# Optimization experiments

Hardware: AMD Instinct MI355X
Metric: run time of the kernel (lower is better)

## Reference

```python
import jax, jax.numpy as jnp
import numpy as np

B, INPUTS, HIDDEN, OUTPUTS = 128, 512, 512, 512
MAXLEN = INPUTS  # required by the module's bmm/cat shape constraints


def setup_inputs() -> dict:
    key = jax.random.key(0)
    ks = jax.random.split(key, 11)
    s = 0.03
    return {
        "x": jax.random.normal(ks[0], (B, INPUTS, MAXLEN), jnp.float32),
        "attn_W": jax.random.normal(ks[1], (MAXLEN, HIDDEN + INPUTS), jnp.float32) * s,
        "attn_b": jax.random.normal(ks[2], (MAXLEN,), jnp.float32) * s,
        "comb_W": jax.random.normal(ks[3], (HIDDEN, INPUTS + MAXLEN), jnp.float32) * s,
        "comb_b": jax.random.normal(ks[4], (HIDDEN,), jnp.float32) * s,
        "w_ih": jax.random.normal(ks[5], (3 * HIDDEN, HIDDEN), jnp.float32) * s,
        "w_hh": jax.random.normal(ks[6], (3 * HIDDEN, HIDDEN), jnp.float32) * s,
        "b_ih": jax.random.normal(ks[7], (3 * HIDDEN,), jnp.float32) * s,
        "b_hh": jax.random.normal(ks[8], (3 * HIDDEN,), jnp.float32) * s,
        "out_W": jax.random.normal(ks[9], (OUTPUTS, HIDDEN), jnp.float32) * s,
        "out_b": jax.random.normal(ks[10], (OUTPUTS,), jnp.float32) * s,
    }


def reference(x, attn_W, attn_b, comb_W, comb_b, w_ih, w_hh, b_ih, b_hh, out_W, out_b):
    # x: [B, inputs, T] with T == max_length == inputs (shape constraint of the module).
    # The torch code loops over batch with identical per-element math -> vectorize over B,
    # and uses lax.scan over the sequential time dimension.
    Bn = x.shape[0]
    H = w_hh.shape[1]
    xs = jnp.moveaxis(x, 2, 0)  # [T, B, inputs]
    h0 = jnp.zeros((Bn, H), x.dtype)

    def step(h, inp):
        # inp: [B, inputs], h: [B, hidden]
        cat = jnp.concatenate([inp, h], axis=1)                     # [B, inputs+hidden]
        attn_w = jax.nn.softmax(cat @ attn_W.T + attn_b, axis=1)    # [B, max_length]
        applied = jnp.einsum('bm,bmt->bt', attn_w, x)               # [B, T]
        g = jnp.concatenate([inp, applied], axis=1) @ comb_W.T + comb_b
        g = jax.nn.relu(g)                                          # [B, hidden]
        # PyTorch GRU cell
        gi = g @ w_ih.T + b_ih
        gh = h @ w_hh.T + b_hh
        ir, iz, i_n = jnp.split(gi, 3, axis=1)
        hr, hz, h_n = jnp.split(gh, 3, axis=1)
        r = jax.nn.sigmoid(ir + hr)
        z = jax.nn.sigmoid(iz + hz)
        n = jnp.tanh(i_n + r * h_n)
        h_new = (1.0 - z) * n + z * h
        return h_new, None

    h_final, _ = jax.lax.scan(step, h0, xs)
    return h_final @ out_W.T + out_b  # [B, outputs]
```

## Files before the change

### kernel.cpp

```cpp
#include <hip/hip_runtime.h>


typedef unsigned short u16;
typedef unsigned int u32;
typedef _Float16 h2 __attribute__((ext_vector_type(2)));
typedef _Float16 f16x8 __attribute__((ext_vector_type(8)));
typedef float f32x4 __attribute__((ext_vector_type(4)));
typedef float f32x2 __attribute__((ext_vector_type(2)));
typedef u32 u32x4 __attribute__((ext_vector_type(4)));

#define MAGIC 0x13579BDFu

#define OFF_AW   65536
#define OFF_CW   1114112
#define OFF_WIH  2162688
#define OFF_WHH  3735552
#define OFF_OW   5308416
#define OFF_HB   5832704
#define OFF_SF   5963776
#define OFF_AP0  6225920
#define OFF_AP1  6488064
#define OFF_GB   6750208
#define OFF_GH   6881280
#define OFF_XT   7667712
#define WS_NEED  74776576

#define FS_S   64
#define FS_C   96
#define FS_G   128
#define FS_GH  160
#define FS_H   192
#define FS_RDY 224

__device__ __forceinline__ float sigmoidf_(float v) { return 1.f / (1.f + __expf(-v)); }
__device__ __forceinline__ float tanhf_(float v) {
  v = fminf(fmaxf(v, -15.f), 15.f);
  float e2 = __expf(2.f * v);
  return (e2 - 1.f) / (e2 + 1.f);
}
__device__ __forceinline__ u32 packh2(float a, float b) {
  h2 v; v.x = (_Float16)a; v.y = (_Float16)b;
  return __builtin_bit_cast(u32, v);
}

__device__ __forceinline__ void vm_drain() { asm volatile("s_waitcnt vmcnt(0)" ::: "memory"); }

__device__ __forceinline__ f32x2 ldg_f32x2(const void* p) {
  f32x2 r;
  asm volatile("global_load_dwordx2 %0, %1, off sc0 sc1\n\ts_waitcnt vmcnt(0)"
               : "=v"(r) : "v"(p) : "memory");
  return r;
}
__device__ __forceinline__ void ldg4x16_off(const void* p, u32x4& a, u32x4& b, u32x4& c, u32x4& d) {
  asm volatile(
      "global_load_dwordx4 %0, %4, off sc0 sc1\n\t"
      "global_load_dwordx4 %1, %4, off offset:16 sc0 sc1\n\t"
      "global_load_dwordx4 %2, %4, off offset:32 sc0 sc1\n\t"
      "global_load_dwordx4 %3, %4, off offset:48 sc0 sc1\n\t"
      "s_waitcnt vmcnt(0)"
      : "=&v"(a), "=&v"(b), "=&v"(c), "=&v"(d)
      : "v"(p) : "memory");
}
__device__ __forceinline__ void ldg_ap16(const float* pa, const float* pb,
                                         u32x4 (&A)[8], u32x4 (&B)[8]) {
  asm volatile(
      "global_load_dwordx4 %0, %16, off sc0 sc1\n\t"
      "global_load_dwordx4 %1, %16, off offset:16 sc0 sc1\n\t"
      "global_load_dwordx4 %2, %16, off offset:32 sc0 sc1\n\t"
      "global_load_dwordx4 %3, %16, off offset:48 sc0 sc1\n\t"
      "global_load_dwordx4 %4, %16, off offset:64 sc0 sc1\n\t"
      "global_load_dwordx4 %5, %16, off offset:80 sc0 sc1\n\t"
      "global_load_dwordx4 %6, %16, off offset:96 sc0 sc1\n\t"
      "global_load_dwordx4 %7, %16, off offset:112 sc0 sc1\n\t"
      "global_load_dwordx4 %8, %17, off sc0 sc1\n\t"
      "global_load_dwordx4 %9, %17, off offset:16 sc0 sc1\n\t"
      "global_load_dwordx4 %10, %17, off offset:32 sc0 sc1\n\t"
      "global_load_dwordx4 %11, %17, off offset:48 sc0 sc1\n\t"
      "global_load_dwordx4 %12, %17, off offset:64 sc0 sc1\n\t"
      "global_load_dwordx4 %13, %17, off offset:80 sc0 sc1\n\t"
      "global_load_dwordx4 %14, %17, off offset:96 sc0 sc1\n\t"
      "global_load_dwordx4 %15, %17, off offset:112 sc0 sc1\n\t"
      "s_waitcnt vmcnt(0)"
      : "=&v"(A[0]), "=&v"(A[1]), "=&v"(A[2]), "=&v"(A[3]),
        "=&v"(A[4]), "=&v"(A[5]), "=&v"(A[6]), "=&v"(A[7]),
        "=&v"(B[0]), "=&v"(B[1]), "=&v"(B[2]), "=&v"(B[3]),
        "=&v"(B[4]), "=&v"(B[5]), "=&v"(B[6]), "=&v"(B[7])
      : "v"(pa), "v"(pb) : "memory");
}
__device__ __forceinline__ void ldg_gh12(const float* q0, const float* q1,
                                         const float* q2, const float* q3,
                                         float (&rr)[4], float (&zz)[4], float (&nn)[4]) {
  asm volatile(
      "global_load_dword %0, %12, off offset:-2048 sc0 sc1\n\t"
      "global_load_dword %4, %12, off sc0 sc1\n\t"
      "global_load_dword %8, %12, off offset:2048 sc0 sc1\n\t"
      "global_load_dword %1, %13, off offset:-2048 sc0 sc1\n\t"
      "global_load_dword %5, %13, off sc0 sc1\n\t"
      "global_load_dword %9, %13, off offset:2048 sc0 sc1\n\t"
      "global_load_dword %2, %14, off offset:-2048 sc0 sc1\n\t"
      "global_load_dword %6, %14, off sc0 sc1\n\t"
      "global_load_dword %10, %14, off offset:2048 sc0 sc1\n\t"
      "global_load_dword %3, %15, off offset:-2048 sc0 sc1\n\t"
      "global_load_dword %7, %15, off sc0 sc1\n\t"
      "global_load_dword %11, %15, off offset:2048 sc0 sc1\n\t"
      "s_waitcnt vmcnt(0)"
      : "=&v"(rr[0]), "=&v"(rr[1]), "=&v"(rr[2]), "=&v"(rr[3]),
        "=&v"(zz[0]), "=&v"(zz[1]), "=&v"(zz[2]), "=&v"(zz[3]),
        "=&v"(nn[0]), "=&v"(nn[1]), "=&v"(nn[2]), "=&v"(nn[3])
      : "v"(q0), "v"(q1), "v"(q2), "v"(q3) : "memory");
}

__device__ __forceinline__ void stg_f32(float* p, float v) {
  asm volatile("global_store_dword %0, %1, off sc0 sc1" :: "v"(p), "v"(v) : "memory");
}
__device__ __forceinline__ void stg_f32x2(float* p, f32x2 v) {
  asm volatile("global_store_dwordx2 %0, %1, off sc0 sc1" :: "v"(p), "v"(v) : "memory");
}
__device__ __forceinline__ void stg_u16(u16* p, u32 v) {
  asm volatile("global_store_short %0, %1, off sc0 sc1" :: "v"(p), "v"(v) : "memory");
}

__device__ __forceinline__ void flag_add(u32* ctrl, int fs) {
  vm_drain();
  __syncthreads();
  if (threadIdx.x == 0) atomicAdd(ctrl + fs, 1u);
}
__device__ __forceinline__ void flag_wait_ge(u32* ctrl, int fs, u32 target, int warp) {
  if (warp == 0) {
    u32 v;
    do {
      v = __hip_atomic_load(ctrl + fs, __ATOMIC_RELAXED, __HIP_MEMORY_SCOPE_AGENT);
    } while (v < target);
  }
  __syncthreads();
}

__device__ __forceinline__ void stage_rows(const u16* gsrc, char* lds, int tid) {
  const int row = tid >> 4, c = tid & 15;
  const u16* g = gsrc + row * 512 + c * 32;
  u32x4 a, b, cc, d;
  ldg4x16_off(g, a, b, cc, d);
  u32x4* dst = (u32x4*)(lds + row * 1040 + c * 64);
  dst[0] = a; dst[1] = b; dst[2] = cc; dst[3] = d;
}

#define MFMA(a, b, c) __builtin_amdgcn_mfma_f32_16x16x32_f16((a), (b), (c), 0, 0, 0)

extern "C" __global__ void __launch_bounds__(256, 1)
rnn_fused(const float* __restrict__ x, const float* __restrict__ attn_W,
          const float* __restrict__ attn_b, const float* __restrict__ comb_W,
          const float* __restrict__ comb_b, const float* __restrict__ w_ih,
          const float* __restrict__ w_hh, const float* __restrict__ b_ih,
          const float* __restrict__ b_hh, const float* __restrict__ out_W,
          const float* __restrict__ out_b, float* __restrict__ out,
          char* __restrict__ ws)
{
  const int tid  = threadIdx.x;
  const int lane = tid & 63;
  const int warp = tid >> 6;

  int team, tb;
  {
    const int r = blockIdx.x & 7;
    const int s = blockIdx.x >> 3;
    if (s < 16) {
      if (r < 4) { team = r * 2 + (s >> 3); tb = s & 7; }
      else       { team = (r - 4) * 2 + (s >> 3); tb = 8 + (s & 7); }
    } else {
      team = r; tb = s;
    }
  }

  const int tt   = tb * 256 + tid;
  const int gb0  = team * 16;
  const int lb   = tb >> 1;
  const int half = tb & 1;
  const int b    = gb0 + lb;
  const int m0h  = half * 256;

  u32* ctrl = (u32*)ws + team * 1024;

  u16*   AW  = (u16*)(ws + OFF_AW);
  u16*   CW  = (u16*)(ws + OFF_CW);
  u16*   WIH = (u16*)(ws + OFF_WIH);
  u16*   WHH = (u16*)(ws + OFF_WHH);
  u16*   OW  = (u16*)(ws + OFF_OW);
  u16*   HB  = (u16*)(ws + OFF_HB);
  float* Sf  = (float*)(ws + OFF_SF);
  float* AP0 = (float*)(ws + OFF_AP0);
  float* AP1 = (float*)(ws + OFF_AP1);
  u16*   GB  = (u16*)(ws + OFF_GB);
  float* GH  = (float*)(ws + OFF_GH);
  u16*   XT  = (u16*)(ws + OFF_XT);

  __shared__ char smem[16704];
  float*     tbuf   = (float*)smem;
  u32*       pLDS   = (u32*)smem;
  float*     redbuf = (float*)(smem + 512);
  float*     rbuf   = (float*)(smem + 8704);
  _Float16*  ldsF   = (_Float16*)smem;

  if (tb == 0) {
    for (int i = 1 + tid; i < 1024; i += 256) ctrl[i] = 0u;
    __syncthreads();
    if (tid == 0) { __threadfence(); atomicExch(ctrl, MAGIC); }
  }
  if (tid == 0) {
    while (__hip_atomic_load(ctrl, __ATOMIC_RELAXED, __HIP_MEMORY_SCOPE_AGENT) != MAGIC) {}
    __threadfence();
  }
  __syncthreads();

  for (int i = tt; i < 512 * 1024; i += 8192) AW[i]  = __builtin_bit_cast(u16, (_Float16)attn_W[i]);
  for (int i = tt; i < 512 * 1024; i += 8192) CW[i]  = __builtin_bit_cast(u16, (_Float16)comb_W[i]);
  for (int i = tt; i < 1536 * 512; i += 8192) WIH[i] = __builtin_bit_cast(u16, (_Float16)w_ih[i]);
  for (int i = tt; i < 1536 * 512; i += 8192) WHH[i] = __builtin_bit_cast(u16, (_Float16)w_hh[i]);
  for (int i = tt; i < 512 * 512;  i += 8192) OW[i]  = __builtin_bit_cast(u16, (_Float16)out_W[i]);
  HB[(size_t)gb0 * 512 + tt] = 0;

  {
    const float* xb  = x  + (size_t)b * 512 * 512;
    u16*         xtB = XT + (size_t)b * 512 * 512;
    for (int mt = 0; mt < 4; ++mt) {
      for (int ct = 0; ct < 8; ++ct) {
        for (int rr = warp; rr < 64; rr += 4)
          tbuf[rr * 65 + lane] = xb[(size_t)(m0h + mt * 64 + rr) * 512 + ct * 64 + lane];
        __syncthreads();
        for (int rr = warp; rr < 64; rr += 4)
          xtB[(size_t)(ct * 64 + rr) * 512 + m0h + mt * 64 + lane] =
              __builtin_bit_cast(u16, (_Float16)tbuf[lane * 65 + rr]);
        __syncthreads();
      }
    }
  }

  vm_drain();
  __syncthreads();
  if (tid == 0) { __threadfence(); atomicAdd(ctrl + FS_RDY, 1u); }
  flag_wait_ge(ctrl, FS_RDY, 32u, warp);
  __threadfence();

  uint4 xr4[64];
  {
    const u16* base = XT + (size_t)b * 262144 + m0h + warp * 64;
#pragma unroll
    for (int r = 0; r < 8; ++r) {
      const uint4* row = (const uint4*)(base + (size_t)(lane * 8 + r) * 512);
#pragma unroll
      for (int jj = 0; jj < 8; ++jj) xr4[r * 8 + jj] = row[jj];
    }
  }

  const int  r16 = lane & 15, q = lane >> 4, q8 = q * 8;
  const bool isA = (tb < 8), isW = (tb >= 8 && tb < 16);
  const int  W4 = ((tb < 8) ? tb : tb - 8) * 4 + warp;
  const int  n0 = W4 * 16;

  float biasA = 0.f, biasD = 0.f, biasI0 = 0.f, biasI1 = 0.f, biasI2 = 0.f,
        biasH0 = 0.f, biasH1 = 0.f, biasH2 = 0.f, biasO = 0.f;
  if (isA) {
    biasA = attn_b[n0 + r16]; biasD = comb_b[n0 + r16];
    biasI0 = b_ih[n0 + r16]; biasI1 = b_ih[512 + n0 + r16]; biasI2 = b_ih[1024 + n0 + r16];
    biasO = out_b[n0 + r16];
  }
  if (isW) {
    biasH0 = b_hh[n0 + r16]; biasH1 = b_hh[512 + n0 + r16]; biasH2 = b_hh[1024 + n0 + r16];
  }

  float hreg[4] = {0.f, 0.f, 0.f, 0.f};

  for (int t = 0; t < 512; ++t) {
    const u32 tok = (u32)(t + 1);

    if (isA) {
      flag_wait_ge(ctrl, FS_H, 8u * (u32)t, warp);
      stage_rows(HB + gb0 * 512, smem, tid);
      __syncthreads();
      f32x4 acc = {0.f, 0.f, 0.f, 0.f};
      const u16* aXp = XT + (size_t)(gb0 + r16) * 262144 + (size_t)t * 512 + q8;
      const _Float16* aHl = ldsF + r16 * 520 + q8;
      const u16* bWp = AW + (size_t)(n0 + r16) * 1024 + q8;
#pragma unroll 4
      for (int k0 = 0; k0 < 512; k0 += 32)
        acc = MFMA(*(const f16x8*)(aXp + k0), *(const f16x8*)(bWp + k0), acc);
#pragma unroll 4
      for (int k0 = 0; k0 < 512; k0 += 32)
        acc = MFMA(*(const f16x8*)(aHl + k0), *(const f16x8*)(bWp + 512 + k0), acc);
#pragma unroll
      for (int i = 0; i < 4; ++i)
        stg_f32(Sf + (size_t)(gb0 + q * 4 + i) * 512 + n0 + r16, acc[i] + biasA);
      flag_add(ctrl, FS_S);
    } else if (isW) {
      flag_wait_ge(ctrl, FS_H, 8u * (u32)t, warp);
      stage_rows(HB + gb0 * 512, smem, tid);
      __syncthreads();
      f32x4 a0 = {0.f,0.f,0.f,0.f}, a1 = {0.f,0.f,0.f,0.f}, a2 = {0.f,0.f,0.f,0.f};
      const _Float16* aHl = ldsF + r16 * 520 + q8;
      const u16* b0p = WHH + (size_t)(n0 + r16) * 512 + q8;
      const u16* b1p = WHH + (size_t)(512 + n0 + r16) * 512 + q8;
      const u16* b2p = WHH + (size_t)(1024 + n0 + r16) * 512 + q8;
#pragma unroll 4
      for (int k0 = 0; k0 < 512; k0 += 32) {
        f16x8 a = *(const f16x8*)(aHl + k0);
        a0 = MFMA(a, *(const f16x8*)(b0p + k0), a0);
        a1 = MFMA(a, *(const f16x8*)(b1p + k0), a1);
        a2 = MFMA(a, *(const f16x8*)(b2p + k0), a2);
      }
#pragma unroll
      for (int i = 0; i < 4; ++i) {
        const size_t ro = (size_t)(gb0 + q * 4 + i) * 1536;
        stg_f32(GH + ro + n0 + r16,        a0[i] + biasH0);
        stg_f32(GH + ro + 512 + n0 + r16,  a1[i] + biasH1);
        stg_f32(GH + ro + 1024 + n0 + r16, a2[i] + biasH2);
      }
      flag_add(ctrl, FS_GH);
    }

    flag_wait_ge(ctrl, FS_S, 8u * tok, warp);
    {
      const int tc = 2 * tid;
      f32x2 sv = ldg_f32x2(Sf + (size_t)b * 512 + tc);
      float s0 = sv.x, s1 = sv.y;
      float mx = fmaxf(s0, s1);
#pragma unroll
      for (int off = 32; off; off >>= 1) mx = fmaxf(mx, __shfl_xor(mx, off, 64));
      if (lane == 0) rbuf[warp] = mx;
      __syncthreads();
      mx = fmaxf(fmaxf(rbuf[0], rbuf[1]), fmaxf(rbuf[2], rbuf[3]));
      float e0 = __expf(s0 - mx), e1 = __expf(s1 - mx);
      float sm = e0 + e1;
#pragma unroll
      for (int off = 32; off; off >>= 1) sm += __shfl_xor(sm, off, 64);
      if (lane == 0) rbuf[4 + warp] = sm;
      __syncthreads();
      sm = rbuf[4] + rbuf[5] + rbuf[6] + rbuf[7];
      const float inv = 1.f / sm;
      if ((tid >> 7) == half) {
        pLDS[tid & 127] = packh2(e0 * inv, e1 * inv);
      }
      __syncthreads();

      uint4 pz4[8];
      const uint4* pp = (const uint4*)pLDS + warp * 8;
#pragma unroll
      for (int jj = 0; jj < 8; ++jj) pz4[jj] = pp[jj];
      float accr[8];
#pragma unroll
      for (int r = 0; r < 8; ++r) {
        h2 sA = {(_Float16)0.f, (_Float16)0.f};
        h2 sB = {(_Float16)0.f, (_Float16)0.f};
#pragma unroll
        for (int jj = 0; jj < 8; ++jj) {
          uint4 xw = xr4[r * 8 + jj], pw = pz4[jj];
          sA = __builtin_bit_cast(h2, xw.x) * __builtin_bit_cast(h2, pw.x) + sA;
          sB = __builtin_bit_cast(h2, xw.y) * __builtin_bit_cast(h2, pw.y) + sB;
          sA = __builtin_bit_cast(h2, xw.z) * __builtin_bit_cast(h2, pw.z) + sA;
          sB = __builtin_bit_cast(h2, xw.w) * __builtin_bit_cast(h2, pw.w) + sB;
        }
        accr[r] = (float)sA.x + (float)sA.y + (float)sB.x + (float)sB.y;
      }
#pragma unroll
      for (int r = 0; r < 8; ++r) redbuf[warp * 512 + lane * 8 + r] = accr[r];
      __syncthreads();
      {
        float v0 = redbuf[tc]     + redbuf[512 + tc]     + redbuf[1024 + tc]     + redbuf[1536 + tc];
        float v1 = redbuf[tc + 1] + redbuf[512 + tc + 1] + redbuf[1024 + tc + 1] + redbuf[1536 + tc + 1];
        float* dst = (half ? AP1 : AP0) + (size_t)b * 512 + tc;
        f32x2 vv; vv.x = v0; vv.y = v1;
        stg_f32x2(dst, vv);
      }
      flag_add(ctrl, FS_C);
    }

    if (isA) {
      f32x4 acc = {0.f, 0.f, 0.f, 0.f};
      const u16* aXp = XT + (size_t)(gb0 + r16) * 262144 + (size_t)t * 512 + q8;
      const u16* bWp = CW + (size_t)(n0 + r16) * 1024 + q8;
#pragma unroll 4
      for (int k0 = 0; k0 < 512; k0 += 32)
        acc = MFMA(*(const f16x8*)(aXp + k0), *(const f16x8*)(bWp + k0), acc);
      flag_wait_ge(ctrl, FS_C, 32u * tok, warp);
      {
        const int row = tid >> 4, c = tid & 15;
        const float* g0 = AP0 + (size_t)(gb0 + row) * 512 + c * 32;
        const float* g1 = AP1 + (size_t)(gb0 + row) * 512 + c * 32;
        u32* dst = (u32*)(smem + row * 1040 + c * 64);
        u32x4 A[8], B[8];
        ldg_ap16(g0, g1, A, B);
#pragma unroll
        for (int k = 0; k < 8; ++k) {
          f32x4 s = __builtin_bit_cast(f32x4, A[k]) + __builtin_bit_cast(f32x4, B[k]);
          dst[2 * k]     = packh2(s[0], s[1]);
          dst[2 * k + 1] = packh2(s[2], s[3]);
        }
      }
      __syncthreads();
      const _Float16* aAl = ldsF + r16 * 520 + q8;
#pragma unroll 4
      for (int k0 = 0; k0 < 512; k0 += 32)
        acc = MFMA(*(const f16x8*)(aAl + k0), *(const f16x8*)(bWp + 512 + k0), acc);
#pragma unroll
      for (int i = 0; i < 4; ++i) {
        float g = fmaxf(acc[i] + biasD, 0.f);
        stg_u16(GB + (size_t)(gb0 + q * 4 + i) * 512 + n0 + r16,
                (u32)__builtin_bit_cast(u16, (_Float16)g));
      }
      flag_add(ctrl, FS_G);
      flag_wait_ge(ctrl, FS_G, 8u * tok, warp);
      stage_rows(GB + gb0 * 512, smem, tid);
      __syncthreads();

      f32x4 g0 = {0.f,0.f,0.f,0.f}, g1 = {0.f,0.f,0.f,0.f}, g2 = {0.f,0.f,0.f,0.f};
      const _Float16* aGl = ldsF + r16 * 520 + q8;
      const u16* w0p = WIH + (size_t)(n0 + r16) * 512 + q8;
      const u16* w1p = WIH + (size_t)(512 + n0 + r16) * 512 + q8;
      const u16* w2p = WIH + (size_t)(1024 + n0 + r16) * 512 + q8;
#pragma unroll 4
      for (int k0 = 0; k0 < 512; k0 += 32) {
        f16x8 a = *(const f16x8*)(aGl + k0);
        g0 = MFMA(a, *(const f16x8*)(w0p + k0), g0);
        g1 = MFMA(a, *(const f16x8*)(w1p + k0), g1);
        g2 = MFMA(a, *(const f16x8*)(w2p + k0), g2);
      }
      flag_wait_ge(ctrl, FS_GH, 8u * tok, warp);
      {
        const int j = n0 + r16;
        const float* q0p = GH + (size_t)(gb0 + q * 4 + 0) * 1536 + 512 + j;
        const float* q1p = GH + (size_t)(gb0 + q * 4 + 1) * 1536 + 512 + j;
        const float* q2p = GH + (size_t)(gb0 + q * 4 + 2) * 1536 + 512 + j;
        const float* q3p = GH + (size_t)(gb0 + q * 4 + 3) * 1536 + 512 + j;
        float ghr[4], ghz[4], ghn[4];
        ldg_gh12(q0p, q1p, q2p, q3p, ghr, ghz, ghn);
#pragma unroll
        for (int i = 0; i < 4; ++i) {
          const int bi = gb0 + q * 4 + i;
          float gir = g0[i] + biasI0, giz = g1[i] + biasI1, gin = g2[i] + biasI2;
          float rg = sigmoidf_(gir + ghr[i]);
          float zg = sigmoidf_(giz + ghz[i]);
          float ng = tanhf_(gin + rg * ghn[i]);
          hreg[i] = (1.f - zg) * ng + zg * hreg[i];
          stg_u16(HB + (size_t)bi * 512 + j,
                  (u32)__builtin_bit_cast(u16, (_Float16)hreg[i]));
        }
      }
      flag_add(ctrl, FS_H);
    }
  }

  if (isA) {
    flag_wait_ge(ctrl, FS_H, 8u * 512u, warp);
    stage_rows(HB + gb0 * 512, smem, tid);
    __syncthreads();
    f32x4 acc = {0.f, 0.f, 0.f, 0.f};
    const _Float16* aHl = ldsF + r16 * 520 + q8;
    const u16* bOp = OW + (size_t)(n0 + r16) * 512 + q8;
#pragma unroll 4
    for (int k0 = 0; k0 < 512; k0 += 32)
      acc = MFMA(*(const f16x8*)(aHl + k0), *(const f16x8*)(bOp + k0), acc);
#pragma unroll
    for (int i = 0; i < 4; ++i)
      out[(size_t)(gb0 + q * 4 + i) * 512 + n0 + r16] = acc[i] + biasO;
  }
}

extern "C" void kernel_launch(void* const* d_in, const int* in_sizes, int n_in,
                              void* d_out, int out_size, void* d_ws, size_t ws_size,
                              hipStream_t stream) {
  if (ws_size < (size_t)WS_NEED) return;
  rnn_fused<<<dim3(256), dim3(256), 0, stream>>>(
      (const float*)d_in[0], (const float*)d_in[1], (const float*)d_in[2],
      (const float*)d_in[3], (const float*)d_in[4], (const float*)d_in[5],
      (const float*)d_in[6], (const float*)d_in[7], (const float*)d_in[8],
      (const float*)d_in[9], (const float*)d_in[10],
      (float*)d_out, (char*)d_ws);
}
```

Before: 18.65 ms.

## Prefetch next timestep's x tile into registers and stage it in LDS

The attention-side blocks now load the x tile for step t+1 into registers alongside the softmax score load, then write it to a second LDS buffer at the start of the next step. Both the attention and combine MFMA loops read x from LDS instead of streaming it from global memory on every k-iteration. This takes global-load latency off the serial recurrence's critical path. In exchange it doubles shared memory per block and holds 16 extra VGPRs across the step.

```diff
diff --git a/kernel.cpp b/kernel.cpp
--- a/kernel.cpp
+++ b/kernel.cpp
@@ -60,6 +60,28 @@
       "s_waitcnt vmcnt(0)"
       : "=&v"(a), "=&v"(b), "=&v"(c), "=&v"(d)
       : "v"(p) : "memory");
+}
+__device__ __forceinline__ void ldg4x16_wait(const void* p, u32x4& a, u32x4& b, u32x4& c, u32x4& d) {
+  asm volatile(
+      "global_load_dwordx4 %0, %4, off\n\t"
+      "global_load_dwordx4 %1, %4, off offset:16\n\t"
+      "global_load_dwordx4 %2, %4, off offset:32\n\t"
+      "global_load_dwordx4 %3, %4, off offset:48\n\t"
+      "s_waitcnt vmcnt(0)"
+      : "=&v"(a), "=&v"(b), "=&v"(c), "=&v"(d)
+      : "v"(p) : "memory");
+}
+__device__ __forceinline__ void ldg_sf_x(const float* sp, const u16* xp, f32x2& sv,
+                                         u32x4& a, u32x4& b, u32x4& c, u32x4& d) {
+  asm volatile(
+      "global_load_dwordx2 %0, %5, off sc0 sc1\n\t"
+      "global_load_dwordx4 %1, %6, off\n\t"
+      "global_load_dwordx4 %2, %6, off offset:16\n\t"
+      "global_load_dwordx4 %3, %6, off offset:32\n\t"
+      "global_load_dwordx4 %4, %6, off offset:48\n\t"
+      "s_waitcnt vmcnt(0)"
+      : "=&v"(sv), "=&v"(a), "=&v"(b), "=&v"(c), "=&v"(d)
+      : "v"(sp), "v"(xp) : "memory");
 }
 __device__ __forceinline__ void ldg_ap16(const float* pa, const float* pb,
                                          u32x4 (&A)[8], u32x4 (&B)[8]) {
@@ -193,12 +215,13 @@
   float* GH  = (float*)(ws + OFF_GH);
   u16*   XT  = (u16*)(ws + OFF_XT);
 
-  __shared__ char smem[16704];
+  __shared__ char smem[33408];
   float*     tbuf   = (float*)smem;
   u32*       pLDS   = (u32*)smem;
   float*     redbuf = (float*)(smem + 512);
   float*     rbuf   = (float*)(smem + 8704);
   _Float16*  ldsF   = (_Float16*)smem;
+  _Float16*  xldsF  = (_Float16*)(smem + 16768);
 
   if (tb == 0) {
     for (int i = 1 + tid; i < 1024; i += 256) ctrl[i] = 0u;
@@ -267,6 +290,13 @@
     biasH0 = b_hh[n0 + r16]; biasH1 = b_hh[512 + n0 + r16]; biasH2 = b_hh[1024 + n0 + r16];
   }
 
+  u32x4 xp0, xp1, xp2, xp3;
+  const int xrow = tid >> 4, xc = tid & 15;
+  if (isA) {
+    const u16* gp = XT + (size_t)(gb0 + xrow) * 262144 + xc * 32;
+    ldg4x16_wait(gp, xp0, xp1, xp2, xp3);
+  }
+
   float hreg[4] = {0.f, 0.f, 0.f, 0.f};
 
   for (int t = 0; t < 512; ++t) {
@@ -274,15 +304,19 @@
 
     if (isA) {
       flag_wait_ge(ctrl, FS_H, 8u * (u32)t, warp);
+      {
+        u32x4* dst = (u32x4*)((char*)xldsF + xrow * 1040 + xc * 64);
+        dst[0] = xp0; dst[1] = xp1; dst[2] = xp2; dst[3] = xp3;
+      }
       stage_rows(HB + gb0 * 512, smem, tid);
       __syncthreads();
       f32x4 acc = {0.f, 0.f, 0.f, 0.f};
-      const u16* aXp = XT + (size_t)(gb0 + r16) * 262144 + (size_t)t * 512 + q8;
+      const _Float16* aXl = xldsF + r16 * 520 + q8;
       const _Float16* aHl = ldsF + r16 * 520 + q8;
       const u16* bWp = AW + (size_t)(n0 + r16) * 1024 + q8;
 #pragma unroll 4
       for (int k0 = 0; k0 < 512; k0 += 32)
-        acc = MFMA(*(const f16x8*)(aXp + k0), *(const f16x8*)(bWp + k0), acc);
+        acc = MFMA(*(const f16x8*)(aXl + k0), *(const f16x8*)(bWp + k0), acc);
 #pragma unroll 4
       for (int k0 = 0; k0 < 512; k0 += 32)
         acc = MFMA(*(const f16x8*)(aHl + k0), *(const f16x8*)(bWp + 512 + k0), acc);
@@ -319,7 +353,14 @@
     flag_wait_ge(ctrl, FS_S, 8u * tok, warp);
     {
       const int tc = 2 * tid;
-      f32x2 sv = ldg_f32x2(Sf + (size_t)b * 512 + tc);
+      f32x2 sv;
+      if (isA) {
+        const int tp = (t < 511) ? t + 1 : t;
+        const u16* gp = XT + (size_t)(gb0 + xrow) * 262144 + (size_t)tp * 512 + xc * 32;
+        ldg_sf_x(Sf + (size_t)b * 512 + tc, gp, sv, xp0, xp1, xp2, xp3);
+      } else {
+        sv = ldg_f32x2(Sf + (size_t)b * 512 + tc);
+      }
       float s0 = sv.x, s1 = sv.y;
       float mx = fmaxf(s0, s1);
 #pragma unroll
@@ -374,11 +415,11 @@
 
     if (isA) {
       f32x4 acc = {0.f, 0.f, 0.f, 0.f};
-      const u16* aXp = XT + (size_t)(gb0 + r16) * 262144 + (size_t)t * 512 + q8;
+      const _Float16* aXl = xldsF + r16 * 520 + q8;
       const u16* bWp = CW + (size_t)(n0 + r16) * 1024 + q8;
 #pragma unroll 4
       for (int k0 = 0; k0 < 512; k0 += 32)
-        acc = MFMA(*(const f16x8*)(aXp + k0), *(const f16x8*)(bWp + k0), acc);
+        acc = MFMA(*(const f16x8*)(aXl + k0), *(const f16x8*)(bWp + k0), acc);
       flag_wait_ge(ctrl, FS_C, 32u * tok, warp);
       {
         const int row = tid >> 4, c = tid & 15;
```

Result: faster. 17.71 ms (-5.0%).
